# Kernel tuning notes

Measured on AMD Instinct MI355X. Metric: run time of the kernel, lower is better.

## Reference

```python
import jax, jax.numpy as jnp
import numpy as np

T, E, DIM, HID = 8192, 8, 1024, 2048


def setup_inputs() -> dict:
    key = jax.random.key(0)
    k1, k2, k3 = jax.random.split(key, 3)
    x = jax.random.normal(k1, (T, DIM), dtype=jnp.float32)
    w1 = jax.random.normal(k2, (E, HID, DIM), dtype=jnp.float32)
    w2 = jax.random.normal(k3, (E, DIM, HID), dtype=jnp.float32)
    # Tokens are pre-grouped by expert; counts must sum exactly to T.
    num_tokens_per_expert = jnp.full((E,), T // E, dtype=jnp.int32)
    return {"x": x, "w1": w1, "w2": w2, "num_tokens_per_expert": num_tokens_per_expert}


def reference(x, w1, w2, num_tokens_per_expert):
    # Faithful to torch._grouped_mm path: bf16 casts, two ragged grouped GEMMs,
    # result cast back to x.dtype.
    gs = num_tokens_per_expert.astype(jnp.int32)
    xb = x.astype(jnp.bfloat16)                                  # [T, dim]
    w1t = jnp.swapaxes(w1.astype(jnp.bfloat16), -2, -1)          # [E, dim, hid]
    w2t = jnp.swapaxes(w2.astype(jnp.bfloat16), -2, -1)          # [E, hid, dim]
    h = jax.lax.ragged_dot(xb, w1t, gs)                          # [T, hid] bf16
    out = jax.lax.ragged_dot(h, w2t, gs)                         # [T, dim] bf16
    return out.astype(x.dtype)
```

## Files before the change

kernel.cpp:

```cpp
#include <hip/hip_runtime.h>
#include <stdint.h>

#define T_TOK 8192
#define NEXP  8
#define DIMSZ 1024
#define HIDSZ 2048

typedef __attribute__((ext_vector_type(4))) float f32x4;
typedef __attribute__((ext_vector_type(8))) short s16x8;


__device__ __forceinline__ uint16_t f2bf(float f) {
  uint32_t u = __builtin_bit_cast(uint32_t, f);
  u += 0x7fffu + ((u >> 16) & 1u);
  return (uint16_t)(u >> 16);
}

__device__ __forceinline__ void gload_lds16(const uint16_t* g, const uint16_t* lds_base) {
  __builtin_amdgcn_global_load_lds(
      (const __attribute__((address_space(1))) uint32_t*)(uintptr_t)g,
      (__attribute__((address_space(3))) uint32_t*)(uint32_t)(uintptr_t)lds_base,
      16, 0, 0);
}


__global__ void cvt_all(const float* __restrict__ x, const float* __restrict__ w1,
                        const float* __restrict__ w2, uint16_t* __restrict__ xb,
                        uint16_t* __restrict__ w1b, uint16_t* __restrict__ w2b,
                        const int* __restrict__ counts, int* __restrict__ offs,
                        int* __restrict__ toffs) {
  if (blockIdx.x == 0 && threadIdx.x == 0) {
    int s = 0, ts = 0;
    for (int e = 0; e < NEXP; ++e) {
      offs[e] = s; toffs[e] = ts;
      s += counts[e]; ts += (counts[e] + 127) >> 7;
    }
    offs[NEXP] = s; toffs[NEXP] = ts;
  }
  const int NX = (T_TOK * DIMSZ) / 8;
  const int NW = (NEXP * HIDSZ * DIMSZ) / 8;
  const int total = NX + 2 * NW;
  const int stride = gridDim.x * blockDim.x;
  for (int i = blockIdx.x * blockDim.x + threadIdx.x; i < total; i += stride) {
    const float* src; uint16_t* dst; int j;
    if (i < NX)           { src = x;  dst = xb;  j = i; }
    else if (i < NX + NW) { src = w1; dst = w1b; j = i - NX; }
    else                  { src = w2; dst = w2b; j = i - NX - NW; }
    const float4* p = (const float4*)src + 2 * (size_t)j;
    float4 a = p[0], b = p[1];
    uint4 o;
    o.x = f2bf(a.x) | ((uint32_t)f2bf(a.y) << 16);
    o.y = f2bf(a.z) | ((uint32_t)f2bf(a.w) << 16);
    o.z = f2bf(b.x) | ((uint32_t)f2bf(b.y) << 16);
    o.w = f2bf(b.z) | ((uint32_t)f2bf(b.w) << 16);
    ((uint4*)dst)[j] = o;
  }
}

template <bool OUT_BF16>
__global__ __launch_bounds__(256, 4)
void gemm_grouped(const uint16_t* __restrict__ A, const uint16_t* __restrict__ B,
                  void* __restrict__ C, const int* __restrict__ offs,
                  const int* __restrict__ toffs, int N, int K, int lognt) {
  __shared__ __align__(16) uint16_t As[128 * 32];
  __shared__ __align__(16) uint16_t Bs[128 * 32];

  const int mtg = blockIdx.x >> lognt;
  const int nt  = blockIdx.x & ((1 << lognt) - 1);
  if (mtg >= toffs[NEXP]) return;
  int e = 0;
#pragma unroll
  for (int i = 1; i < NEXP; ++i) e += (toffs[i] <= mtg) ? 1 : 0;
  const int mt      = mtg - toffs[e];
  const int m_start = offs[e];
  const int m_count = offs[e + 1] - m_start;
  const int m0      = mt * 128;
  int valid_m = m_count - m0;
  if (valid_m > 128) valid_m = 128;
  const int n0 = nt * 128;

  const int tid  = threadIdx.x;
  const int w    = tid >> 6;
  const int lane = tid & 63;
  const int wm = w & 1, wn = w >> 1;

  const int srow0 = w * 16 + (lane >> 2);
  const int srow1 = (w + 4) * 16 + (lane >> 2);
  const int scol  = (((lane & 3) ^ ((lane >> 3) & 3))) * 8;

  const uint16_t* gA = A + (size_t)m_start * K;
  const uint16_t* gB = B + (size_t)e * N * K;

  const int ar0 = m0 + (srow0 < valid_m ? srow0 : valid_m - 1);
  const int ar1 = m0 + (srow1 < valid_m ? srow1 : valid_m - 1);

  const uint16_t* a0p = gA + (size_t)ar0 * K + scol;
  const uint16_t* a1p = gA + (size_t)ar1 * K + scol;
  const uint16_t* b0p = gB + (size_t)(n0 + srow0) * K + scol;
  const uint16_t* b1p = gB + (size_t)(n0 + srow1) * K + scol;

  const uint16_t* lA0 = &As[w * 512];
  const uint16_t* lA1 = &As[(w + 4) * 512];
  const uint16_t* lB0 = &Bs[w * 512];
  const uint16_t* lB1 = &Bs[(w + 4) * 512];

  const int fr  = lane & 15;
  const int fk  = ((lane >> 4) ^ ((fr >> 1) & 3)) * 8;

  f32x4 acc[4][4];
#pragma unroll
  for (int mi = 0; mi < 4; ++mi)
#pragma unroll
    for (int ni = 0; ni < 4; ++ni) acc[mi][ni] = (f32x4){0.f, 0.f, 0.f, 0.f};

  for (int k0 = 0; k0 < K; k0 += 32) {
    __syncthreads();
    gload_lds16(a0p, lA0);
    gload_lds16(a1p, lA1);
    gload_lds16(b0p, lB0);
    gload_lds16(b1p, lB1);
    a0p += 32; a1p += 32; b0p += 32; b1p += 32;
    __syncthreads();

    s16x8 af[4], bf[4];
#pragma unroll
    for (int mi = 0; mi < 4; ++mi)
      af[mi] = *(const s16x8*)&As[(wm * 64 + mi * 16 + fr) * 32 + fk];
#pragma unroll
    for (int ni = 0; ni < 4; ++ni)
      bf[ni] = *(const s16x8*)&Bs[(wn * 64 + ni * 16 + fr) * 32 + fk];
#pragma unroll
    for (int mi = 0; mi < 4; ++mi)
#pragma unroll
      for (int ni = 0; ni < 4; ++ni)
        acc[mi][ni] = __builtin_amdgcn_mfma_f32_16x16x32_bf16(af[mi], bf[ni], acc[mi][ni], 0, 0, 0);
  }

  const int cq = (lane >> 4) * 4;
  const int cc = lane & 15;
#pragma unroll
  for (int mi = 0; mi < 4; ++mi) {
#pragma unroll
    for (int r = 0; r < 4; ++r) {
      const int rt = wm * 64 + mi * 16 + cq + r;
      if (rt < valid_m) {
        const size_t rowoff = (size_t)(m_start + m0 + rt) * N;
#pragma unroll
        for (int ni = 0; ni < 4; ++ni) {
          const int col = n0 + wn * 64 + ni * 16 + cc;
          const float v = acc[mi][ni][r];
          if (OUT_BF16) {
            ((uint16_t*)C)[rowoff + col] = f2bf(v);
          } else {
            const uint32_t b = (uint32_t)f2bf(v) << 16;
            ((float*)C)[rowoff + col] = __builtin_bit_cast(float, b);
          }
        }
      }
    }
  }
}


extern "C" void kernel_launch(void* const* d_in, const int* in_sizes, int n_in,
                              void* d_out, int out_size, void* d_ws, size_t ws_size,
                              hipStream_t stream) {
  const float* x  = (const float*)d_in[0];
  const float* w1 = (const float*)d_in[1];
  const float* w2 = (const float*)d_in[2];
  const int* cnt  = (const int*)d_in[3];
  float* out = (float*)d_out;

  char* ws = (char*)d_ws;
  uint16_t* xb  = (uint16_t*)(ws);
  uint16_t* w1b = (uint16_t*)(ws + 16777216);
  uint16_t* w2b = (uint16_t*)(ws + 50331648);
  uint16_t* h   = (uint16_t*)(ws + 83886080);
  int* offs     = (int*)(ws + 117440512);
  int* toffs    = offs + 9;

  cvt_all<<<4096, 256, 0, stream>>>(x, w1, w2, xb, w1b, w2b, cnt, offs, toffs);

  const int MAX_MT = T_TOK / 128 + NEXP - 1;

  gemm_grouped<true><<<MAX_MT * 16, 256, 0, stream>>>(
      xb, w1b, (void*)h, offs, toffs, HIDSZ, DIMSZ, 4);

  gemm_grouped<false><<<MAX_MT * 8, 256, 0, stream>>>(
      h, w2b, (void*)out, offs, toffs, DIMSZ, HIDSZ, 3);
}
```

Before: 290.5 us.

## Double GEMM K-tile to 64 with wider swizzle; widen conversion per-thread work

The grouped GEMM now stages a 128x64 K-slice of A and B into LDS per iteration instead of 128x32. The XOR swizzle is widened to 8 chunks to match, and two MFMA sub-steps run per barrier pair, which halves the number of __syncthreads and load rounds. LDS per block doubles to 32 KB and launch bounds drop to 3 blocks per SM, trading occupancy for fewer barriers. The conversion kernel now has each thread handle 16 floats using half as many blocks.

```diff
diff --git a/kernel.cpp b/kernel.cpp
--- a/kernel.cpp
+++ b/kernel.cpp
@@ -37,8 +37,8 @@
     }
     offs[NEXP] = s; toffs[NEXP] = ts;
   }
-  const int NX = (T_TOK * DIMSZ) / 8;
-  const int NW = (NEXP * HIDSZ * DIMSZ) / 8;
+  const int NX = (T_TOK * DIMSZ) / 16;
+  const int NW = (NEXP * HIDSZ * DIMSZ) / 16;
   const int total = NX + 2 * NW;
   const int stride = gridDim.x * blockDim.x;
   for (int i = blockIdx.x * blockDim.x + threadIdx.x; i < total; i += stride) {
@@ -46,24 +46,30 @@
     if (i < NX)           { src = x;  dst = xb;  j = i; }
     else if (i < NX + NW) { src = w1; dst = w1b; j = i - NX; }
     else                  { src = w2; dst = w2b; j = i - NX - NW; }
-    const float4* p = (const float4*)src + 2 * (size_t)j;
-    float4 a = p[0], b = p[1];
-    uint4 o;
-    o.x = f2bf(a.x) | ((uint32_t)f2bf(a.y) << 16);
-    o.y = f2bf(a.z) | ((uint32_t)f2bf(a.w) << 16);
-    o.z = f2bf(b.x) | ((uint32_t)f2bf(b.y) << 16);
-    o.w = f2bf(b.z) | ((uint32_t)f2bf(b.w) << 16);
-    ((uint4*)dst)[j] = o;
+    const float4* p = (const float4*)src + 4 * (size_t)j;
+    float4 a = p[0], b = p[1], c = p[2], d = p[3];
+    uint4 o0, o1;
+    o0.x = f2bf(a.x) | ((uint32_t)f2bf(a.y) << 16);
+    o0.y = f2bf(a.z) | ((uint32_t)f2bf(a.w) << 16);
+    o0.z = f2bf(b.x) | ((uint32_t)f2bf(b.y) << 16);
+    o0.w = f2bf(b.z) | ((uint32_t)f2bf(b.w) << 16);
+    o1.x = f2bf(c.x) | ((uint32_t)f2bf(c.y) << 16);
+    o1.y = f2bf(c.z) | ((uint32_t)f2bf(c.w) << 16);
+    o1.z = f2bf(d.x) | ((uint32_t)f2bf(d.y) << 16);
+    o1.w = f2bf(d.z) | ((uint32_t)f2bf(d.w) << 16);
+    uint4* q = (uint4*)dst + 2 * (size_t)j;
+    q[0] = o0;
+    q[1] = o1;
   }
 }
 
 template <bool OUT_BF16>
-__global__ __launch_bounds__(256, 4)
+__global__ __launch_bounds__(256, 3)
 void gemm_grouped(const uint16_t* __restrict__ A, const uint16_t* __restrict__ B,
                   void* __restrict__ C, const int* __restrict__ offs,
                   const int* __restrict__ toffs, int N, int K, int lognt) {
-  __shared__ __align__(16) uint16_t As[128 * 32];
-  __shared__ __align__(16) uint16_t Bs[128 * 32];
+  __shared__ __align__(16) uint16_t As[128 * 64];
+  __shared__ __align__(16) uint16_t Bs[128 * 64];
 
   const int mtg = blockIdx.x >> lognt;
   const int nt  = blockIdx.x & ((1 << lognt) - 1);
@@ -84,28 +90,22 @@
   const int lane = tid & 63;
   const int wm = w & 1, wn = w >> 1;
 
-  const int srow0 = w * 16 + (lane >> 2);
-  const int srow1 = (w + 4) * 16 + (lane >> 2);
-  const int scol  = (((lane & 3) ^ ((lane >> 3) & 3))) * 8;
-
   const uint16_t* gA = A + (size_t)m_start * K;
   const uint16_t* gB = B + (size_t)e * N * K;
 
-  const int ar0 = m0 + (srow0 < valid_m ? srow0 : valid_m - 1);
-  const int ar1 = m0 + (srow1 < valid_m ? srow1 : valid_m - 1);
+  const uint16_t* ap[4];
+  const uint16_t* bp[4];
+#pragma unroll
+  for (int c = 0; c < 4; ++c) {
+    const int r  = w * 32 + c * 8 + (lane >> 3);
+    const int q8 = ((lane & 7) ^ ((r >> 1) & 7)) * 8;
+    const int ra = (r < valid_m) ? r : (valid_m - 1);
+    ap[c] = gA + (size_t)(m0 + ra) * K + q8;
+    bp[c] = gB + (size_t)(n0 + r) * K + q8;
+  }
 
-  const uint16_t* a0p = gA + (size_t)ar0 * K + scol;
-  const uint16_t* a1p = gA + (size_t)ar1 * K + scol;
-  const uint16_t* b0p = gB + (size_t)(n0 + srow0) * K + scol;
-  const uint16_t* b1p = gB + (size_t)(n0 + srow1) * K + scol;
-
-  const uint16_t* lA0 = &As[w * 512];
-  const uint16_t* lA1 = &As[(w + 4) * 512];
-  const uint16_t* lB0 = &Bs[w * 512];
-  const uint16_t* lB1 = &Bs[(w + 4) * 512];
-
-  const int fr  = lane & 15;
-  const int fk  = ((lane >> 4) ^ ((fr >> 1) & 3)) * 8;
+  const int fr = lane & 15;
+  const int f0 = ((lane >> 4) ^ ((fr >> 1) & 7)) * 8;
 
   f32x4 acc[4][4];
 #pragma unroll
@@ -113,27 +113,33 @@
 #pragma unroll
     for (int ni = 0; ni < 4; ++ni) acc[mi][ni] = (f32x4){0.f, 0.f, 0.f, 0.f};
 
-  for (int k0 = 0; k0 < K; k0 += 32) {
+  for (int k0 = 0; k0 < K; k0 += 64) {
     __syncthreads();
-    gload_lds16(a0p, lA0);
-    gload_lds16(a1p, lA1);
-    gload_lds16(b0p, lB0);
-    gload_lds16(b1p, lB1);
-    a0p += 32; a1p += 32; b0p += 32; b1p += 32;
+#pragma unroll
+    for (int c = 0; c < 4; ++c) {
+      gload_lds16(ap[c], &As[(w * 32 + c * 8) * 64]);
+      gload_lds16(bp[c], &Bs[(w * 32 + c * 8) * 64]);
+    }
+#pragma unroll
+    for (int c = 0; c < 4; ++c) { ap[c] += 64; bp[c] += 64; }
     __syncthreads();
 
-    s16x8 af[4], bf[4];
 #pragma unroll
-    for (int mi = 0; mi < 4; ++mi)
-      af[mi] = *(const s16x8*)&As[(wm * 64 + mi * 16 + fr) * 32 + fk];
+    for (int kk = 0; kk < 2; ++kk) {
+      const int fk = f0 ^ (kk << 5);
+      s16x8 af[4], bf[4];
 #pragma unroll
-    for (int ni = 0; ni < 4; ++ni)
-      bf[ni] = *(const s16x8*)&Bs[(wn * 64 + ni * 16 + fr) * 32 + fk];
-#pragma unroll
-    for (int mi = 0; mi < 4; ++mi)
+      for (int mi = 0; mi < 4; ++mi)
+        af[mi] = *(const s16x8*)&As[(wm * 64 + mi * 16 + fr) * 64 + fk];
 #pragma unroll
       for (int ni = 0; ni < 4; ++ni)
-        acc[mi][ni] = __builtin_amdgcn_mfma_f32_16x16x32_bf16(af[mi], bf[ni], acc[mi][ni], 0, 0, 0);
+        bf[ni] = *(const s16x8*)&Bs[(wn * 64 + ni * 16 + fr) * 64 + fk];
+#pragma unroll
+      for (int mi = 0; mi < 4; ++mi)
+#pragma unroll
+        for (int ni = 0; ni < 4; ++ni)
+          acc[mi][ni] = __builtin_amdgcn_mfma_f32_16x16x32_bf16(af[mi], bf[ni], acc[mi][ni], 0, 0, 0);
+    }
   }
 
   const int cq = (lane >> 4) * 4;
@@ -179,7 +185,7 @@
   int* offs     = (int*)(ws + 117440512);
   int* toffs    = offs + 9;
 
-  cvt_all<<<4096, 256, 0, stream>>>(x, w1, w2, xb, w1b, w2b, cnt, offs, toffs);
+  cvt_all<<<2048, 256, 0, stream>>>(x, w1, w2, xb, w1b, w2b, cnt, offs, toffs);
 
   const int MAX_MT = T_TOK / 128 + NEXP - 1;
 
```

After: 269.9 us. 7.1% less time.
